# Optimization experiments

Hardware: AMD Instinct MI355X
Metric: run time of the kernel (lower is better)

## Reference

```python
import jax, jax.numpy as jnp
import numpy as np

H = 2048
I = 8192
E = 8
EI = I // E  # expert_intermediate_size = 1024


def setup_inputs() -> dict:
    key = jax.random.key(0)
    k1, k2, k3 = jax.random.split(key, 3)
    B, N = 4, 4096
    x = jax.random.normal(k1, (B, N, H), dtype=jnp.float32)
    position_ids = jnp.arange(B * N, dtype=jnp.int64).reshape(B, N)
    gate_up_proj = 0.02 * jax.random.normal(k2, (E, H, EI * 2), dtype=jnp.float32)
    down_proj = 0.02 * jax.random.normal(k3, (E, EI, H), dtype=jnp.float32)
    return {"x": x, "position_ids": position_ids,
            "gate_up_proj": gate_up_proj, "down_proj": down_proj}


def reference(x, position_ids, gate_up_proj, down_proj):
    # x: [B,N,H]; position_ids: [B,N] (or [N]); expert = pos % E.
    B, N, Hdim = x.shape
    if position_ids.ndim == 1:
        position_ids = jnp.broadcast_to(position_ids[None, :], (B, N))
    eids = (position_ids % E).reshape(B * N)
    flat = x.reshape(B * N, Hdim)

    # Modulo routing is perfectly balanced (N % E == 0 with sequential ids),
    # so group tokens by expert (stable sort) and run dense per-expert GEMMs
    # instead of per-token gathered-weight bmm (same math, no weight blowup).
    T = B * N
    order = jnp.argsort(eids)          # stable in jax -> tokens grouped by expert
    xg = flat[order].reshape(E, T // E, Hdim)            # [E, T/E, H]
    gu = jnp.einsum('ebh,ehk->ebk', xg, gate_up_proj)    # [E, T/E, 2*EI]
    gate, up = gu[..., :EI], gu[..., EI:]
    inter = jax.nn.silu(gate) * up                       # [E, T/E, EI]
    outg = jnp.einsum('ebi,eih->ebh', inter, down_proj)  # [E, T/E, H]
    out = jnp.zeros((T, Hdim), dtype=x.dtype).at[order].set(outg.reshape(T, Hdim))
    return out.reshape(B, N, Hdim)
```

## Files before the change

### kernel.cpp

```cpp
#include <hip/hip_runtime.h>
#include <hip/hip_bf16.h>

typedef unsigned short u16;
typedef __attribute__((ext_vector_type(8))) short short8;
typedef __attribute__((ext_vector_type(8))) unsigned short u16x8;
typedef __attribute__((ext_vector_type(4))) float f32x4;

#define H_DIM 2048
#define EI_DIM 1024
#define NEXP 8

template <int V> struct IC { static constexpr int value = V; };

__device__ __forceinline__ u16 f2bf(float f) {
  __hip_bfloat16 h = __float2bfloat16(f);
  return __builtin_bit_cast(unsigned short, h);
}

__device__ __forceinline__ void load_lds16(const void* g, void* lds) {
  __builtin_amdgcn_global_load_lds(
      (const __attribute__((address_space(1))) unsigned int*)g,
      (__attribute__((address_space(3))) unsigned int*)lds, 16, 0, 0);
}

__global__ void hist_kernel(const int* __restrict__ pid, int* __restrict__ hist) {
  int seg = blockIdx.x, lane = threadIdx.x;
  int eid = pid[seg * 64 + lane] & 7;
#pragma unroll
  for (int e = 0; e < NEXP; ++e) {
    unsigned long long m = __ballot(eid == e);
    if (lane == 0) hist[e * 256 + seg] = __popcll(m);
  }
}

__global__ void scan_kernel(const int* __restrict__ hist, int* __restrict__ base,
                            int* __restrict__ offcnt, int T) {
  __shared__ int lds[256];
  int tid = threadIdx.x;
  int v[8], s = 0;
#pragma unroll
  for (int j = 0; j < 8; ++j) { v[j] = hist[tid * 8 + j]; s += v[j]; }
  lds[tid] = s;
  __syncthreads();
  for (int d = 1; d < 256; d <<= 1) {
    int t = (tid >= d) ? lds[tid - d] : 0;
    __syncthreads();
    lds[tid] += t;
    __syncthreads();
  }
  int run = lds[tid] - s;
#pragma unroll
  for (int j = 0; j < 8; ++j) { base[tid * 8 + j] = run; run += v[j]; }
  __syncthreads();
  if (tid < NEXP) {
    int o = base[tid * 256];
    int nx = (tid < NEXP - 1) ? base[(tid + 1) * 256] : T;
    offcnt[tid] = o;
    offcnt[8 + tid] = nx - o;
  }
}

__global__ void rank_kernel(const int* __restrict__ pid, const int* __restrict__ base,
                            int* __restrict__ order) {
  int seg = blockIdx.x, lane = threadIdx.x;
  int t = seg * 64 + lane;
  int eid = pid[t] & 7;
  unsigned long long below = (1ull << lane) - 1ull;
#pragma unroll
  for (int e = 0; e < NEXP; ++e) {
    unsigned long long m = __ballot(eid == e);
    if (eid == e) {
      int r = __popcll(m & below);
      order[base[e * 256 + seg] + r] = t;
    }
  }
}

__global__ __launch_bounds__(256) void transpose_bf16(const float* __restrict__ in,
                                                      u16* __restrict__ out, int R, int C) {
  __shared__ u16 tile[64][65];
  int nbr = R >> 6, nbc = C >> 6;
  int per_e = nbr * nbc;
  int bx = blockIdx.x;
  int e = bx / per_e, rem = bx % per_e;
  int tr = rem % nbr, tc = rem / nbr;
  const float* ine = in + (size_t)e * R * C;
  u16* oute = out + (size_t)e * R * C;
  int r0 = tr * 64, c0 = tc * 64;
  int tid = threadIdx.x;
  int lrow = tid >> 4, lc4 = (tid & 15) * 4;
#pragma unroll
  for (int p = 0; p < 4; ++p) {
    int rl = p * 16 + lrow;
    float4 v = *(const float4*)&ine[(size_t)(r0 + rl) * C + c0 + lc4];
    tile[rl][lc4 + 0] = f2bf(v.x);
    tile[rl][lc4 + 1] = f2bf(v.y);
    tile[rl][lc4 + 2] = f2bf(v.z);
    tile[rl][lc4 + 3] = f2bf(v.w);
  }
  __syncthreads();
#pragma unroll
  for (int p = 0; p < 2; ++p) {
    int idx = p * 256 + tid;
    int jr = idx >> 3, hg = (idx & 7) * 8;
    u16x8 v;
#pragma unroll
    for (int i = 0; i < 8; ++i) v[i] = tile[hg + i][jr];
    *(u16x8*)&oute[(size_t)(c0 + jr) * R + r0 + hg] = v;
  }
}

__global__ __launch_bounds__(256) void gather_x(const float* __restrict__ x,
                                                const int* __restrict__ order,
                                                u16* __restrict__ xg) {
  int g = blockIdx.x;
  int t = order[g];
  const float* src = x + (size_t)t * H_DIM;
  u16* dst = xg + (size_t)g * H_DIM;
  int c = threadIdx.x * 8;
  float4 a = *(const float4*)&src[c];
  float4 b = *(const float4*)&src[c + 4];
  u16x8 v;
  v[0] = f2bf(a.x); v[1] = f2bf(a.y); v[2] = f2bf(a.z); v[3] = f2bf(a.w);
  v[4] = f2bf(b.x); v[5] = f2bf(b.y); v[6] = f2bf(b.z); v[7] = f2bf(b.w);
  *(u16x8*)&dst[c] = v;
}

template <int KTOT, int KIND>
__device__ __forceinline__ void gemm8_body(
    const u16* __restrict__ A, const u16* __restrict__ Bmat, void* __restrict__ outp,
    const int* __restrict__ offcnt, const int* __restrict__ order, int T) {
  constexpr int NK = KTOT / 64;
  constexpr int ASTR = (KIND == 0) ? H_DIM : EI_DIM;
  constexpr int BSTR = ASTR;
  constexpr size_t BEXP = (size_t)2048 * BSTR;
  __shared__ u16 As[2][2][8192];
  __shared__ u16 Bs[2][2][8192];

  int nwg = gridDim.x;
  int bid = blockIdx.x;
  int bx = (bid & 7) * (nwg >> 3) + (bid >> 3);
  int e = bx >> 6;
  int s = bx & 63;
  int off = offcnt[e], cnt = offcnt[8 + e];
  const u16* Be = Bmat + (size_t)e * BEXP;

  int tid = threadIdx.x, w = tid >> 6, l = tid & 63;
  int wm = w >> 2, wn = w & 3, lr = l & 15, lg = l >> 4;
  int cidx = (lg ^ ((lr >> 1) & 3)) * 8;
  int aRow0 = wm * 128 + lr;
  int bRow0 = wn * 64 + lr;
  int sr[2], sc[2];
#pragma unroll
  for (int j = 0; j < 2; ++j) {
    sr[j] = j * 128 + (tid >> 2);
    int c = tid & 3;
    sc[j] = (c ^ ((sr[j] >> 1) & 3)) * 8;
  }

#pragma unroll 1
  for (int it = s; it < 512; it += 64) {
    int mt = it >> 3, nt = it & 7;
    if (mt * 256 >= cnt) continue;

    const u16* aSrc[2];
    const u16* bSrc[2];
#pragma unroll
    for (int j = 0; j < 2; ++j) {
      int r = sr[j];
      int grow = min(off + mt * 256 + r, T - 1);
      aSrc[j] = A + (size_t)grow * ASTR + sc[j];
      int n;
      if (KIND == 0) {
        int q = r >> 4, rr = r & 15;
        n = ((q & 2) ? EI_DIM : 0) + nt * 128 + ((q >> 2) << 5) + ((q & 1) << 4) + rr;
      } else {
        n = nt * 256 + r;
      }
      bSrc[j] = Be + (size_t)n * BSTR + sc[j];
    }

    auto stageA = [&](int kt, int kh, int buf) {
#pragma unroll
      for (int j = 0; j < 2; ++j)
        load_lds16(aSrc[j] + kt * 64 + kh * 32, &As[buf][kh][j * 4096 + w * 512]);
    };
    auto stageB = [&](int kt, int kh, int buf) {
#pragma unroll
      for (int j = 0; j < 2; ++j)
        load_lds16(bSrc[j] + kt * 64 + kh * 32, &Bs[buf][kh][j * 4096 + w * 512]);
    };

    short8 avA[4], avB[4], bvA[4], bvB[4];
    auto RDA = [&](short8(&dst)[4], int buf, int kh, int h) {
#pragma unroll
      for (int mm = 0; mm < 4; ++mm)
        dst[mm] = *(const short8*)&As[buf][kh][(aRow0 + (h * 4 + mm) * 16) * 32 + cidx];
    };
    auto RDB = [&](short8(&dst)[4], int buf, int kh) {
#pragma unroll
      for (int nn = 0; nn < 4; ++nn)
        dst[nn] = *(const short8*)&Bs[buf][kh][(bRow0 + nn * 16) * 32 + cidx];
    };

    f32x4 acc[8][4];
#pragma unroll
    for (int m = 0; m < 8; ++m)
#pragma unroll
      for (int nn = 0; nn < 4; ++nn) acc[m][nn] = {0.f, 0.f, 0.f, 0.f};

    auto MF = [&](short8(&a)[4], short8(&b)[4], auto HC) {
      constexpr int h = decltype(HC)::value;
      __builtin_amdgcn_s_setprio(1);
#pragma unroll
      for (int mm = 0; mm < 4; ++mm)
#pragma unroll
        for (int nn = 0; nn < 4; ++nn)
          acc[h * 4 + mm][nn] =
              __builtin_amdgcn_mfma_f32_16x16x32_bf16(a[mm], b[nn], acc[h * 4 + mm][nn], 0, 0, 0);
      __builtin_amdgcn_s_setprio(0);
    };

    __syncthreads();

    stageA(0, 0, 0); stageB(0, 0, 0); stageA(0, 1, 0); stageB(0, 1, 0);
    stageB(1, 0, 1); stageA(1, 0, 1); stageB(1, 1, 1);
    asm volatile("s_waitcnt vmcnt(6)" ::: "memory");
    __builtin_amdgcn_s_barrier();
    __builtin_amdgcn_sched_barrier(0);

    auto TILE = [&](int t, auto BC) {
      constexpr int b = decltype(BC)::value;
      constexpr int bn = b ^ 1;
      RDA(avA, b, 0, 0);
      RDB(bvA, b, 0);
      stageA(t + 1, 1, bn);
      MF(avA, bvA, IC<0>{});
      RDA(avB, b, 0, 1);
      __builtin_amdgcn_s_barrier();
      stageB(t + 2, 0, b);
      MF(avB, bvA, IC<1>{});
      RDA(avA, b, 1, 0);
      RDB(bvB, b, 1);
      __builtin_amdgcn_s_barrier();
      stageA(t + 2, 0, b);
      MF(avA, bvB, IC<0>{});
      asm volatile("s_waitcnt vmcnt(4)" ::: "memory");
      RDA(avB, b, 1, 1);
      __builtin_amdgcn_s_barrier();
      stageB(t + 2, 1, b);
      MF(avB, bvB, IC<1>{});
      __builtin_amdgcn_s_barrier();
    };

#pragma unroll 1
    for (int t = 0; t < NK - 3; t += 2) {
      TILE(t, IC<0>{});
      TILE(t + 1, IC<1>{});
    }

    {
      RDA(avA, 0, 0, 0);
      RDB(bvA, 0, 0);
      stageA(NK - 1, 1, 1);
      MF(avA, bvA, IC<0>{});
      RDA(avB, 0, 0, 1);
      __builtin_amdgcn_s_barrier();
      MF(avB, bvA, IC<1>{});
      RDA(avA, 0, 1, 0);
      RDB(bvB, 0, 1);
      __builtin_amdgcn_s_barrier();
      MF(avA, bvB, IC<0>{});
      asm volatile("s_waitcnt vmcnt(0)" ::: "memory");
      RDA(avB, 0, 1, 1);
      __builtin_amdgcn_s_barrier();
      MF(avB, bvB, IC<1>{});
      __builtin_amdgcn_s_barrier();
      RDA(avA, 1, 0, 0);
      RDB(bvA, 1, 0);
      MF(avA, bvA, IC<0>{});
      RDA(avB, 1, 0, 1);
      MF(avB, bvA, IC<1>{});
      RDA(avA, 1, 1, 0);
      RDB(bvB, 1, 1);
      MF(avA, bvB, IC<0>{});
      RDA(avB, 1, 1, 1);
      MF(avB, bvB, IC<1>{});
    }

    if (KIND == 0) {
      u16* inter = (u16*)outp;
#pragma unroll
      for (int m = 0; m < 8; ++m)
#pragma unroll
        for (int nn = 0; nn < 2; ++nn) {
          f32x4 g = acc[m][nn], u = acc[m][nn + 2];
          int icol = nt * 128 + wn * 32 + nn * 16 + lr;
#pragma unroll
          for (int j = 0; j < 4; ++j) {
            int r = wm * 128 + m * 16 + lg * 4 + j;
            int grow = mt * 256 + r;
            if (grow < cnt) {
              float gv = g[j];
              float val = (gv / (1.f + __expf(-gv))) * u[j];
              inter[(size_t)(off + grow) * EI_DIM + icol] = f2bf(val);
            }
          }
        }
    } else {
      float* out = (float*)outp;
#pragma unroll
      for (int m = 0; m < 8; ++m)
#pragma unroll
        for (int j = 0; j < 4; ++j) {
          int r = wm * 128 + m * 16 + lg * 4 + j;
          int grow = mt * 256 + r;
          if (grow < cnt) {
            float* orow = out + (size_t)order[off + grow] * H_DIM + nt * 256 + wn * 64 + lr;
#pragma unroll
            for (int nn = 0; nn < 4; ++nn) orow[nn * 16] = acc[m][nn][j];
          }
        }
    }
  }
}

__global__ __launch_bounds__(512, 2) void gemm_gu_kernel(
    const u16* __restrict__ A, const u16* __restrict__ Bmat, void* __restrict__ outp,
    const int* __restrict__ offcnt, int T) {
  gemm8_body<2048, 0>(A, Bmat, outp, offcnt, nullptr, T);
}

__global__ __launch_bounds__(512, 2) void gemm_down_kernel(
    const u16* __restrict__ A, const u16* __restrict__ Bmat, void* __restrict__ outp,
    const int* __restrict__ offcnt, const int* __restrict__ order, int T) {
  gemm8_body<1024, 1>(A, Bmat, outp, offcnt, order, T);
}

extern "C" void kernel_launch(void* const* d_in, const int* in_sizes, int n_in,
                              void* d_out, int out_size, void* d_ws, size_t ws_size,
                              hipStream_t stream) {
  const float* x = (const float*)d_in[0];
  const int* pid = (const int*)d_in[1];
  const float* gup = (const float*)d_in[2];
  const float* dwn = (const float*)d_in[3];
  float* out = (float*)d_out;

  const int T = in_sizes[1];

  char* ws = (char*)d_ws;
  size_t o = 0;
  auto take = [&](size_t b) { size_t r = o; o += (b + 255) & ~(size_t)255; return r; };
  int* offcnt = (int*)(ws + take(32 * 4));
  int* hist = (int*)(ws + take(2048 * 4));
  int* base = (int*)(ws + take(2052 * 4));
  int* order = (int*)(ws + take((size_t)T * 4));
  u16* xg = (u16*)(ws + take((size_t)T * H_DIM * 2));
  u16* wguT = (u16*)(ws + take((size_t)NEXP * 2048 * 2048 * 2));
  u16* wdT = (u16*)(ws + take((size_t)NEXP * 2048 * 1024 * 2));
  u16* inter = (u16*)(ws + take((size_t)T * EI_DIM * 2));

  hist_kernel<<<T / 64, 64, 0, stream>>>(pid, hist);
  scan_kernel<<<1, 256, 0, stream>>>(hist, base, offcnt, T);
  rank_kernel<<<T / 64, 64, 0, stream>>>(pid, base, order);
  transpose_bf16<<<NEXP * 32 * 32, 256, 0, stream>>>(gup, wguT, 2048, 2048);
  transpose_bf16<<<NEXP * 16 * 32, 256, 0, stream>>>(dwn, wdT, 1024, 2048);
  gather_x<<<T, 256, 0, stream>>>(x, order, xg);

  gemm_gu_kernel<<<512, 512, 0, stream>>>(xg, wguT, inter, offcnt, T);
  gemm_down_kernel<<<512, 512, 0, stream>>>(inter, wdT, out, offcnt, order, T);
}
```

Before: 335.5 us.

## Merge routing into one block kernel and fuse weight transposes with token gather

Replaces the three routing kernels (histogram, scan, rank) with a single 1024-thread block that keeps the histogram and bases in shared memory. The two weight-transpose kernels and the token gather are merged into one launch, partitioned by block index, and each gather block now handles 8 rows. This cuts launch count from 8 to 4 and drops global round-trips for the histogram and base arrays, removing launch gaps and tail effects. The cost is that routing now runs in a single block on one CU, serialising 16 segments per wave.

Result: no change. 338.4 us (+0.9%).

```diff
diff --git a/kernel.cpp b/kernel.cpp
--- a/kernel.cpp
+++ b/kernel.cpp
@@ -23,65 +23,68 @@
       (__attribute__((address_space(3))) unsigned int*)lds, 16, 0, 0);
 }
 
-__global__ void hist_kernel(const int* __restrict__ pid, int* __restrict__ hist) {
-  int seg = blockIdx.x, lane = threadIdx.x;
-  int eid = pid[seg * 64 + lane] & 7;
-#pragma unroll
-  for (int e = 0; e < NEXP; ++e) {
-    unsigned long long m = __ballot(eid == e);
-    if (lane == 0) hist[e * 256 + seg] = __popcll(m);
-  }
-}
-
-__global__ void scan_kernel(const int* __restrict__ hist, int* __restrict__ base,
-                            int* __restrict__ offcnt, int T) {
+__global__ __launch_bounds__(1024) void route_kernel(const int* __restrict__ pid,
+                                                     int* __restrict__ offcnt,
+                                                     int* __restrict__ order, int T) {
+  __shared__ int hist[2048];
   __shared__ int lds[256];
-  int tid = threadIdx.x;
+  __shared__ int basel[2048];
+  int tid = threadIdx.x, w = tid >> 6, lane = tid & 63;
+  unsigned long long below = (1ull << lane) - 1ull;
+#pragma unroll 1
+  for (int i = 0; i < 16; ++i) {
+    int seg = w * 16 + i;
+    int eid = pid[seg * 64 + lane] & 7;
+#pragma unroll
+    for (int e = 0; e < NEXP; ++e) {
+      unsigned long long m = __ballot(eid == e);
+      if (lane == 0) hist[e * 256 + seg] = __popcll(m);
+    }
+  }
+  __syncthreads();
   int v[8], s = 0;
-#pragma unroll
-  for (int j = 0; j < 8; ++j) { v[j] = hist[tid * 8 + j]; s += v[j]; }
-  lds[tid] = s;
+  if (tid < 256) {
+#pragma unroll
+    for (int j = 0; j < 8; ++j) { v[j] = hist[tid * 8 + j]; s += v[j]; }
+    lds[tid] = s;
+  }
   __syncthreads();
   for (int d = 1; d < 256; d <<= 1) {
-    int t = (tid >= d) ? lds[tid - d] : 0;
+    int t = (tid < 256 && tid >= d) ? lds[tid - d] : 0;
     __syncthreads();
-    lds[tid] += t;
+    if (tid < 256) lds[tid] += t;
     __syncthreads();
   }
-  int run = lds[tid] - s;
-#pragma unroll
-  for (int j = 0; j < 8; ++j) { base[tid * 8 + j] = run; run += v[j]; }
+  if (tid < 256) {
+    int run = lds[tid] - s;
+#pragma unroll
+    for (int j = 0; j < 8; ++j) { basel[tid * 8 + j] = run; run += v[j]; }
+  }
   __syncthreads();
   if (tid < NEXP) {
-    int o = base[tid * 256];
-    int nx = (tid < NEXP - 1) ? base[(tid + 1) * 256] : T;
+    int o = basel[tid * 256];
+    int nx = (tid < NEXP - 1) ? basel[(tid + 1) * 256] : T;
     offcnt[tid] = o;
     offcnt[8 + tid] = nx - o;
   }
-}
-
-__global__ void rank_kernel(const int* __restrict__ pid, const int* __restrict__ base,
-                            int* __restrict__ order) {
-  int seg = blockIdx.x, lane = threadIdx.x;
-  int t = seg * 64 + lane;
-  int eid = pid[t] & 7;
-  unsigned long long below = (1ull << lane) - 1ull;
-#pragma unroll
-  for (int e = 0; e < NEXP; ++e) {
-    unsigned long long m = __ballot(eid == e);
-    if (eid == e) {
-      int r = __popcll(m & below);
-      order[base[e * 256 + seg] + r] = t;
-    }
-  }
-}
-
-__global__ __launch_bounds__(256) void transpose_bf16(const float* __restrict__ in,
-                                                      u16* __restrict__ out, int R, int C) {
+#pragma unroll 1
+  for (int i = 0; i < 16; ++i) {
+    int seg = w * 16 + i;
+    int t = seg * 64 + lane;
+    int eid = pid[t] & 7;
+#pragma unroll
+    for (int e = 0; e < NEXP; ++e) {
+      unsigned long long m = __ballot(eid == e);
+      if (eid == e) order[basel[e * 256 + seg] + __popcll(m & below)] = t;
+    }
+  }
+}
+
+__device__ __forceinline__ void transpose_tile(const float* __restrict__ in,
+                                               u16* __restrict__ out, int R, int C, int bx) {
   __shared__ u16 tile[64][65];
-  int nbr = R >> 6, nbc = C >> 6;
-  int per_e = nbr * nbc;
-  int bx = blockIdx.x;
+  int nbr = R >> 6;
+  int per_e = nbr * (C >> 6);
   int e = bx / per_e, rem = bx % per_e;
   int tr = rem % nbr, tc = rem / nbr;
   const float* ine = in + (size_t)e * R * C;
@@ -110,20 +113,32 @@
   }
 }
 
-__global__ __launch_bounds__(256) void gather_x(const float* __restrict__ x,
-                                                const int* __restrict__ order,
-                                                u16* __restrict__ xg) {
-  int g = blockIdx.x;
-  int t = order[g];
-  const float* src = x + (size_t)t * H_DIM;
-  u16* dst = xg + (size_t)g * H_DIM;
-  int c = threadIdx.x * 8;
-  float4 a = *(const float4*)&src[c];
-  float4 b = *(const float4*)&src[c + 4];
-  u16x8 v;
-  v[0] = f2bf(a.x); v[1] = f2bf(a.y); v[2] = f2bf(a.z); v[3] = f2bf(a.w);
-  v[4] = f2bf(b.x); v[5] = f2bf(b.y); v[6] = f2bf(b.z); v[7] = f2bf(b.w);
-  *(u16x8*)&dst[c] = v;
+__global__ __launch_bounds__(256) void convert_kernel(
+    const float* __restrict__ gup, const float* __restrict__ dwn, const float* __restrict__ x,
+    const int* __restrict__ order, u16* __restrict__ wguT, u16* __restrict__ wdT,
+    u16* __restrict__ xg) {
+  int bx = blockIdx.x;
+  if (bx < 8192) {
+    transpose_tile(gup, wguT, 2048, 2048, bx);
+  } else if (bx < 8192 + 4096) {
+    transpose_tile(dwn, wdT, 1024, 2048, bx - 8192);
+  } else {
+    int g0 = (bx - 12288) * 8;
+    int c = threadIdx.x * 8;
+#pragma unroll 1
+    for (int r = 0; r < 8; ++r) {
+      int g = g0 + r;
+      int t = order[g];
+      const float* src = x + (size_t)t * H_DIM;
+      u16* dst = xg + (size_t)g * H_DIM;
+      float4 a = *(const float4*)&src[c];
+      float4 b = *(const float4*)&src[c + 4];
+      u16x8 vv;
+      vv[0] = f2bf(a.x); vv[1] = f2bf(a.y); vv[2] = f2bf(a.z); vv[3] = f2bf(a.w);
+      vv[4] = f2bf(b.x); vv[5] = f2bf(b.y); vv[6] = f2bf(b.z); vv[7] = f2bf(b.w);
+      *(u16x8*)&dst[c] = vv;
+    }
+  }
 }
 
 template <int KTOT, int KIND>
@@ -352,21 +367,14 @@
   size_t o = 0;
   auto take = [&](size_t b) { size_t r = o; o += (b + 255) & ~(size_t)255; return r; };
   int* offcnt = (int*)(ws + take(32 * 4));
-  int* hist = (int*)(ws + take(2048 * 4));
-  int* base = (int*)(ws + take(2052 * 4));
   int* order = (int*)(ws + take((size_t)T * 4));
   u16* xg = (u16*)(ws + take((size_t)T * H_DIM * 2));
   u16* wguT = (u16*)(ws + take((size_t)NEXP * 2048 * 2048 * 2));
   u16* wdT = (u16*)(ws + take((size_t)NEXP * 2048 * 1024 * 2));
   u16* inter = (u16*)(ws + take((size_t)T * EI_DIM * 2));
 
-  hist_kernel<<<T / 64, 64, 0, stream>>>(pid, hist);
-  scan_kernel<<<1, 256, 0, stream>>>(hist, base, offcnt, T);
-  rank_kernel<<<T / 64, 64, 0, stream>>>(pid, base, order);
-  transpose_bf16<<<NEXP * 32 * 32, 256, 0, stream>>>(gup, wguT, 2048, 2048);
-  transpose_bf16<<<NEXP * 16 * 32, 256, 0, stream>>>(dwn, wdT, 1024, 2048);
-  gather_x<<<T, 256, 0, stream>>>(x, order, xg);
-
+  route_kernel<<<1, 1024, 0, stream>>>(pid, offcnt, order, T);
+  convert_kernel<<<8192 + 4096 + 2048, 256, 0, stream>>>(gup, dwn, x, order, wguT, wdT, xg);
   gemm_gu_kernel<<<512, 512, 0, stream>>>(xg, wguT, inter, offcnt, T);
   gemm_down_kernel<<<512, 512, 0, stream>>>(inter, wdT, out, offcnt, order, T);
 }
```
